# Performance work log

Measured on AMD Instinct MI355X. Metric: run time of the kernel, lower is better.

Reference implementation:

```python
import jax, jax.numpy as jnp
import numpy as np

B, N, D, H = 1, 4096, 512, 8
HD = D // H


def setup_inputs() -> dict:
    key = jax.random.key(0)
    ks = jax.random.split(key, 12)
    s = 0.02  # weight init scale for numerical stability
    query = jax.random.normal(ks[0], (B, N, D), jnp.float32)
    key_t = jax.random.normal(ks[1], (B, N, D), jnp.float32)
    value = jax.random.normal(ks[2], (B, N, D), jnp.float32)
    Wq = jax.random.normal(ks[3], (D, D), jnp.float32) * s
    bq = jax.random.normal(ks[4], (D,), jnp.float32) * s
    Wk = jax.random.normal(ks[5], (D, D), jnp.float32) * s
    bk = jax.random.normal(ks[6], (D,), jnp.float32) * s
    Wv = jax.random.normal(ks[7], (D, D), jnp.float32) * s
    bv = jax.random.normal(ks[8], (D,), jnp.float32) * s
    Wo = jax.random.normal(ks[9], (D, D), jnp.float32) * s
    bo = jax.random.normal(ks[10], (D,), jnp.float32) * s
    # build sgconv_mat exactly as __init__: shifted nonneg adjacency, max-normalized,
    # then symmetric degree normalization D^-1/2 A D^-1/2 (gwmha_layer_num=1)
    A = jax.random.uniform(ks[11], (N, N), jnp.float32)
    A = A + A.min()
    A = A / A.max()
    deg = A.sum(1)
    dinv = 1.0 / jnp.sqrt(deg)
    sgconv_mat = (dinv[:, None] * A * dinv[None, :])[None]  # [1,N,N]
    return {"query": query, "key": key_t, "value": value,
            "Wq": Wq, "bq": bq, "Wk": Wk, "bk": bk, "Wv": Wv, "bv": bv,
            "Wo": Wo, "bo": bo, "sgconv_mat": sgconv_mat}


def reference(query, key, value, Wq, bq, Wk, bk, Wv, bv, Wo, bo, sgconv_mat):
    b, n, d = query.shape
    q = (query @ Wq.T + bq).reshape(b, n, H, HD)
    k = (key @ Wk.T + bk).reshape(b, n, H, HD)
    v = (value @ Wv.T + bv).reshape(b, n, H, HD)
    energy = jnp.einsum('bqhd,bkhd->bhqk', q, k)
    attn = jax.nn.softmax(energy / jnp.sqrt(jnp.float32(d)), axis=3)
    out = jnp.einsum('bhqk,bkhd->bqhd', attn, v).reshape(b, n, d)
    out = sgconv_mat @ out          # [1,N,N] @ [B,N,D] -> [B,N,D]
    return out @ Wo.T + bo
```

## Files before the change

kernel.cpp:

```cpp
#include <hip/hip_runtime.h>
#include <hip/hip_bf16.h>
#include <math.h>

typedef __bf16 bf16_t;
typedef __bf16 bf16x8 __attribute__((ext_vector_type(8)));
typedef unsigned short ushort8v __attribute__((ext_vector_type(8)));
typedef float floatx4 __attribute__((ext_vector_type(4)));

static __device__ inline unsigned short f2bf_rne(float f) {
    unsigned int u = __builtin_bit_cast(unsigned int, f);
    unsigned int r = u + 0x7FFFu + ((u >> 16) & 1u);
    return (unsigned short)(r >> 16);
}
static __device__ inline bf16_t f2bf(float f) {
    return __builtin_bit_cast(bf16_t, f2bf_rne(f));
}

static __device__ inline bf16x8 load8(const bf16_t* p) { return *(const bf16x8*)p; }
static __device__ inline bf16x8 load8(const float* p) {
    float4 a = *(const float4*)p;
    float4 b = *(const float4*)(p + 4);
    ushort8v u;
    u[0] = f2bf_rne(a.x); u[1] = f2bf_rne(a.y); u[2] = f2bf_rne(a.z); u[3] = f2bf_rne(a.w);
    u[4] = f2bf_rne(b.x); u[5] = f2bf_rne(b.y); u[6] = f2bf_rne(b.z); u[7] = f2bf_rne(b.w);
    return __builtin_bit_cast(bf16x8, u);
}
static __device__ inline bf16x8 load8sum(const float* p0, const float* p1) {
    float4 a = *(const float4*)p0;       float4 b = *(const float4*)(p0 + 4);
    float4 c = *(const float4*)p1;       float4 d = *(const float4*)(p1 + 4);
    ushort8v u;
    u[0] = f2bf_rne(a.x + c.x); u[1] = f2bf_rne(a.y + c.y);
    u[2] = f2bf_rne(a.z + c.z); u[3] = f2bf_rne(a.w + c.w);
    u[4] = f2bf_rne(b.x + d.x); u[5] = f2bf_rne(b.y + d.y);
    u[6] = f2bf_rne(b.z + d.z); u[7] = f2bf_rne(b.w + d.w);
    return __builtin_bit_cast(bf16x8, u);
}

static __device__ inline void store_c(float* C, size_t i, float v) { C[i] = v; }
static __device__ inline void store_c(bf16_t* C, size_t i, float v) { C[i] = f2bf(v); }

template <bool ASUM, typename TA, typename TB, typename TC>
__device__ inline void gemm_body(
    const TA* __restrict__ A, const float* __restrict__ A2, int lda,
    const TB* __restrict__ B, int ldb,
    const float* __restrict__ bias_col, const float* __restrict__ bias_row,
    TC* __restrict__ C, int ldc, int K, int m0, int n0)
{
    __shared__ bf16_t As[128 * 40];
    __shared__ bf16_t Bs[64 * 40];

    const int tid = threadIdx.x;
    const int lane = tid & 63, wave = tid >> 6;
    const int wm = wave & 1, wn = wave >> 1;
    const int lo16 = lane & 15, quad = lane >> 4;
    const int sr = tid >> 2, sc = (tid & 3) * 8;

    floatx4 acc[4][2] = {};

    for (int k0 = 0; k0 < K; k0 += 32) {
        bf16x8 a0, a1, b0;
        const size_t ia0 = (size_t)(m0 + sr) * lda + k0 + sc;
        const size_t ia1 = (size_t)(m0 + 64 + sr) * lda + k0 + sc;
        if (ASUM) {
            a0 = load8sum((const float*)A + ia0, A2 + ia0);
            a1 = load8sum((const float*)A + ia1, A2 + ia1);
        } else {
            a0 = load8(A + ia0);
            a1 = load8(A + ia1);
        }
        b0 = load8(B + (size_t)(n0 + sr) * ldb + k0 + sc);
        __syncthreads();
        *(bf16x8*)(&As[sr * 40 + sc]) = a0;
        *(bf16x8*)(&As[(64 + sr) * 40 + sc]) = a1;
        *(bf16x8*)(&Bs[sr * 40 + sc]) = b0;
        __syncthreads();

        bf16x8 af[4], bfv[2];
#pragma unroll
        for (int mt = 0; mt < 4; ++mt)
            af[mt] = *(const bf16x8*)(&As[(wm * 64 + mt * 16 + lo16) * 40 + quad * 8]);
#pragma unroll
        for (int nt = 0; nt < 2; ++nt)
            bfv[nt] = *(const bf16x8*)(&Bs[(wn * 32 + nt * 16 + lo16) * 40 + quad * 8]);
#pragma unroll
        for (int mt = 0; mt < 4; ++mt)
#pragma unroll
            for (int nt = 0; nt < 2; ++nt)
                acc[mt][nt] = __builtin_amdgcn_mfma_f32_16x16x32_bf16(
                    af[mt], bfv[nt], acc[mt][nt], 0, 0, 0);
    }

#pragma unroll
    for (int nt = 0; nt < 2; ++nt) {
        const int gn = n0 + wn * 32 + nt * 16 + lo16;
        const float bc = bias_col ? bias_col[gn] : 0.f;
#pragma unroll
        for (int mt = 0; mt < 4; ++mt) {
#pragma unroll
            for (int r = 0; r < 4; ++r) {
                const int gm = m0 + wm * 64 + mt * 16 + quad * 4 + r;
                float v = acc[mt][nt][r] + bc;
                if (bias_row) v += bias_row[gm];
                store_c(C, (size_t)gm * ldc + gn, v);
            }
        }
    }
}

__global__ __launch_bounds__(256) void proj_qkv(
    const float* __restrict__ query, const float* __restrict__ Wq, const float* __restrict__ bq,
    const float* __restrict__ key,   const float* __restrict__ Wk, const float* __restrict__ bk,
    const float* __restrict__ Wv,    const float* __restrict__ value, const float* __restrict__ bv,
    bf16_t* __restrict__ q, bf16_t* __restrict__ k, bf16_t* __restrict__ vt)
{
    const int b = blockIdx.x;
    const float *A, *B, *bc = nullptr, *br = nullptr;
    bf16_t* C;
    int ldc = 512, m0, n0;
    if (b < 512) {
        int i = b & 255, x = i & 7, t = i >> 3;
        n0 = (t & 7) * 64;
        m0 = ((t >> 3) * 8 + x) * 128;
        if (b < 256) { A = query; B = Wq; bc = bq; C = q; }
        else         { A = key;   B = Wk; bc = bk; C = k; }
    } else {
        int i = b - 512;
        n0 = (i & 63) * 64;
        m0 = (i >> 6) * 128;
        A = Wv; B = value; br = bv; C = vt; ldc = 4096;
    }
    gemm_body<false, float, float, bf16_t>(A, nullptr, 512, B, 512, bc, br, C, ldc, 512, m0, n0);
}

__global__ __launch_bounds__(256) void sgconv_gemm(
    const float* __restrict__ sg, const bf16_t* __restrict__ aot, float* __restrict__ part)
{
    const int b = blockIdx.x;
    const int kb = b >> 8;
    const int i = b & 255, x = i & 7, t = i >> 3;
    const int n0 = (t & 7) * 64, m0 = ((t >> 3) * 8 + x) * 128;
    gemm_body<false, float, bf16_t, float>(
        sg + kb * 2048, nullptr, 4096, aot + kb * 2048, 4096,
        nullptr, nullptr, part + (size_t)kb * 4096 * 512, 512, 2048, m0, n0);
}

__global__ __launch_bounds__(256) void out_proj(
    const float* __restrict__ p0, const float* __restrict__ p1,
    const float* __restrict__ Wo, const float* __restrict__ bo, float* __restrict__ out)
{
    const int i = blockIdx.x, x = i & 7, t = i >> 3;
    const int n0 = (t & 7) * 64, m0 = ((t >> 3) * 8 + x) * 128;
    gemm_body<true, float, float, float>(p0, p1, 512, Wo, 512, bo, nullptr, out, 512, 512, m0, n0);
}

__global__ __launch_bounds__(256, 4) void flash_attn(
    const bf16_t* __restrict__ q, const bf16_t* __restrict__ kk,
    const bf16_t* __restrict__ vt, float* __restrict__ op,
    float* __restrict__ lp, float scale)
{
    const int N = 4096, D = 512;
    const int h   = blockIdx.x & 7;
    const int qb  = (blockIdx.x >> 3) & 31;
    const int qtr = blockIdx.x >> 8;
    const int t0  = qtr * 1024;

    const int tid = threadIdx.x;
    const int w = tid >> 6, lane = tid & 63;
    const int lo16 = lane & 15, quad = lane >> 4;

    __shared__ bf16_t Ks[64 * 72];
    __shared__ bf16_t Vs[64 * 72];
    __shared__ bf16_t Ps[4][32 * 72];

    const bf16_t* qp = q + (size_t)(qb * 128 + w * 32 + lo16) * D + h * 64 + quad * 8;
    bf16x8 qf[2][2];
    qf[0][0] = *(const bf16x8*)qp;
    qf[0][1] = *(const bf16x8*)(qp + 32);
    qf[1][0] = *(const bf16x8*)(qp + 16 * D);
    qf[1][1] = *(const bf16x8*)(qp + 16 * D + 32);

    const int srow = tid >> 2, sc = (tid & 3) * 16;
    const bf16_t* ksrc = kk + (size_t)(t0 + srow) * D + h * 64 + sc;
    const bf16_t* vsrc = vt + (size_t)(h * 64 + srow) * N + t0 + sc;
    bf16_t* kdst = &Ks[srow * 72 + sc];
    bf16_t* vdst = &Vs[srow * 72 + sc];

    floatx4 o[4][2] = {};
    float l[2] = {0.f, 0.f};

    bf16x8 kr0 = *(const bf16x8*)ksrc;
    bf16x8 kr1 = *(const bf16x8*)(ksrc + 8);
    bf16x8 vr0 = *(const bf16x8*)vsrc;
    bf16x8 vr1 = *(const bf16x8*)(vsrc + 8);

    for (int it = 0; it < 16; ++it) {
        __syncthreads();
        *(bf16x8*)kdst = kr0;  *(bf16x8*)(kdst + 8) = kr1;
        *(bf16x8*)vdst = vr0;  *(bf16x8*)(vdst + 8) = vr1;
        __syncthreads();
        if (it < 15) {
            const bf16_t* kn = ksrc + (size_t)(it + 1) * 64 * D;
            const bf16_t* vn = vsrc + (it + 1) * 64;
            kr0 = *(const bf16x8*)kn;  kr1 = *(const bf16x8*)(kn + 8);
            vr0 = *(const bf16x8*)vn;  vr1 = *(const bf16x8*)(vn + 8);
        }

        floatx4 s[4][2];
#pragma unroll
        for (int tt = 0; tt < 4; ++tt) {
            bf16x8 kf0 = *(const bf16x8*)(&Ks[(tt * 16 + lo16) * 72 + quad * 8]);
            bf16x8 kf1 = *(const bf16x8*)(&Ks[(tt * 16 + lo16) * 72 + 32 + quad * 8]);
#pragma unroll
            for (int qt = 0; qt < 2; ++qt) {
                floatx4 a = {};
                a = __builtin_amdgcn_mfma_f32_16x16x32_bf16(kf0, qf[qt][0], a, 0, 0, 0);
                a = __builtin_amdgcn_mfma_f32_16x16x32_bf16(kf1, qf[qt][1], a, 0, 0, 0);
                s[tt][qt] = a;
            }
        }
#pragma unroll
        for (int tt = 0; tt < 4; ++tt)
#pragma unroll
            for (int qt = 0; qt < 2; ++qt) {
                float e0 = __expf(s[tt][qt][0] * scale);
                float e1 = __expf(s[tt][qt][1] * scale);
                float e2 = __expf(s[tt][qt][2] * scale);
                float e3 = __expf(s[tt][qt][3] * scale);
                l[qt] += (e0 + e1) + (e2 + e3);
                uint2 pk;
                pk.x = (unsigned)f2bf_rne(e0) | ((unsigned)f2bf_rne(e1) << 16);
                pk.y = (unsigned)f2bf_rne(e2) | ((unsigned)f2bf_rne(e3) << 16);
                *(uint2*)(&Ps[w][(qt * 16 + lo16) * 72 + tt * 16 + quad * 4]) = pk;
            }
#pragma unroll
        for (int ks = 0; ks < 2; ++ks) {
            bf16x8 pf0 = *(const bf16x8*)(&Ps[w][lo16 * 72 + ks * 32 + quad * 8]);
            bf16x8 pf1 = *(const bf16x8*)(&Ps[w][(16 + lo16) * 72 + ks * 32 + quad * 8]);
#pragma unroll
            for (int t = 0; t < 4; ++t) {
                bf16x8 vf = *(const bf16x8*)(&Vs[(t * 16 + lo16) * 72 + ks * 32 + quad * 8]);
                o[t][0] = __builtin_amdgcn_mfma_f32_16x16x32_bf16(vf, pf0, o[t][0], 0, 0, 0);
                o[t][1] = __builtin_amdgcn_mfma_f32_16x16x32_bf16(vf, pf1, o[t][1], 0, 0, 0);
            }
        }
    }

#pragma unroll
    for (int qt = 0; qt < 2; ++qt) {
        l[qt] += __shfl_xor(l[qt], 16);
        l[qt] += __shfl_xor(l[qt], 32);
    }

    const int g = blockIdx.x & 255;
    float* opw = op + ((size_t)qtr * 256 + g) * 8192;
#pragma unroll
    for (int t = 0; t < 4; ++t)
#pragma unroll
        for (int pt = 0; pt < 2; ++pt)
#pragma unroll
            for (int r = 0; r < 4; ++r)
                opw[(t * 16 + quad * 4 + r) * 128 + w * 32 + pt * 16 + lo16] = o[t][pt][r];

    if (quad == 0) {
        float* lpw = lp + ((size_t)qtr * 256 + g) * 128;
        lpw[w * 32 + lo16] = l[0];
        lpw[w * 32 + 16 + lo16] = l[1];
    }
}

__global__ __launch_bounds__(256) void attn_combine(
    const float* __restrict__ op, const float* __restrict__ lp, bf16_t* __restrict__ aot)
{
    const int g = blockIdx.x;
    const int h = g & 7, qb = g >> 3;
    const int tid = threadIdx.x;
    __shared__ float ls[128];
    if (tid < 128) {
        float s = 0.f;
#pragma unroll
        for (int qtr = 0; qtr < 4; ++qtr)
            s += lp[((size_t)qtr * 256 + g) * 128 + tid];
        ls[tid] = 1.0f / s;
    }
    __syncthreads();
    const float* b0 = op + (size_t)g * 8192;
    const size_t QS = (size_t)256 * 8192;
#pragma unroll 4
    for (int i = 0; i < 32; ++i) {
        int idx = i * 256 + tid;
        float v = b0[idx] + b0[QS + idx] + b0[2 * QS + idx] + b0[3 * QS + idx];
        int dim = idx >> 7, qc = idx & 127;
        aot[(size_t)(h * 64 + dim) * 4096 + qb * 128 + qc] = f2bf(v * ls[qc]);
    }
}

extern "C" void kernel_launch(void* const* d_in, const int* in_sizes, int n_in,
                              void* d_out, int out_size, void* d_ws, size_t ws_size,
                              hipStream_t stream)
{
    const int N = 4096, D = 512;
    const float* query = (const float*)d_in[0];
    const float* key_t = (const float*)d_in[1];
    const float* value = (const float*)d_in[2];
    const float* Wq = (const float*)d_in[3];
    const float* bq = (const float*)d_in[4];
    const float* Wk = (const float*)d_in[5];
    const float* bk = (const float*)d_in[6];
    const float* Wv = (const float*)d_in[7];
    const float* bv = (const float*)d_in[8];
    const float* Wo = (const float*)d_in[9];
    const float* bo = (const float*)d_in[10];
    const float* sg = (const float*)d_in[11];
    float* out = (float*)d_out;

    bf16_t* q   = (bf16_t*)d_ws;
    bf16_t* kk  = q   + (size_t)N * D;
    bf16_t* vt  = kk  + (size_t)N * D;
    bf16_t* aot = vt  + (size_t)N * D;
    float*  op  = (float*)(aot + (size_t)N * D);
    float*  lp  = op + (size_t)4 * 256 * 8192;
    float*  p0  = op;
    float*  p1  = op + (size_t)N * D;

    const dim3 blk(256);

    proj_qkv<<<768, blk, 0, stream>>>(query, Wq, bq, key_t, Wk, bk, Wv, value, bv, q, kk, vt);

    const float scale = 1.0f / sqrtf((float)D);
    flash_attn<<<1024, blk, 0, stream>>>(q, kk, vt, op, lp, scale);
    attn_combine<<<256, blk, 0, stream>>>(op, lp, aot);

    sgconv_gemm<<<512, blk, 0, stream>>>(sg, aot, p0);
    out_proj<<<256, blk, 0, stream>>>(p0, p1, Wo, bo, out);

    (void)in_sizes; (void)n_in; (void)out_size; (void)ws_size;
}
```

Measured before the change: 299.7 us.

## Pre-convert sgconv matrix to bf16 and retile sgconv GEMM with 4-way split-K

The fp32 sgconv matrix is converted to bf16 by 256 extra blocks appended to the projection launch, so the sgconv GEMM reads half the bytes and skips per-tile conversion. The sgconv GEMM gets its own 128x128 tile kernel with 4-way split-K over 1024-wide chunks, replacing the 128x64 tile with 2-way split. The output projection sums four partial buffers, and the LDS row padding goes from 40 to 68 elements. This trades an extra 64MB-read/32MB-write conversion pass and a wider partial-sum reduction for better reuse and fewer bytes in the big GEMM.

```diff
diff --git a/kernel.cpp b/kernel.cpp
--- a/kernel.cpp
+++ b/kernel.cpp
@@ -25,29 +25,35 @@
     u[4] = f2bf_rne(b.x); u[5] = f2bf_rne(b.y); u[6] = f2bf_rne(b.z); u[7] = f2bf_rne(b.w);
     return __builtin_bit_cast(bf16x8, u);
 }
-static __device__ inline bf16x8 load8sum(const float* p0, const float* p1) {
-    float4 a = *(const float4*)p0;       float4 b = *(const float4*)(p0 + 4);
-    float4 c = *(const float4*)p1;       float4 d = *(const float4*)(p1 + 4);
+static __device__ inline bf16x8 load8sum4(const float* p, size_t s) {
+    float4 a0 = *(const float4*)p,           a1 = *(const float4*)(p + 4);
+    float4 b0 = *(const float4*)(p + s),     b1 = *(const float4*)(p + s + 4);
+    float4 c0 = *(const float4*)(p + 2 * s), c1 = *(const float4*)(p + 2 * s + 4);
+    float4 d0 = *(const float4*)(p + 3 * s), d1 = *(const float4*)(p + 3 * s + 4);
     ushort8v u;
-    u[0] = f2bf_rne(a.x + c.x); u[1] = f2bf_rne(a.y + c.y);
-    u[2] = f2bf_rne(a.z + c.z); u[3] = f2bf_rne(a.w + c.w);
-    u[4] = f2bf_rne(b.x + d.x); u[5] = f2bf_rne(b.y + d.y);
-    u[6] = f2bf_rne(b.z + d.z); u[7] = f2bf_rne(b.w + d.w);
+    u[0] = f2bf_rne((a0.x + b0.x) + (c0.x + d0.x));
+    u[1] = f2bf_rne((a0.y + b0.y) + (c0.y + d0.y));
+    u[2] = f2bf_rne((a0.z + b0.z) + (c0.z + d0.z));
+    u[3] = f2bf_rne((a0.w + b0.w) + (c0.w + d0.w));
+    u[4] = f2bf_rne((a1.x + b1.x) + (c1.x + d1.x));
+    u[5] = f2bf_rne((a1.y + b1.y) + (c1.y + d1.y));
+    u[6] = f2bf_rne((a1.z + b1.z) + (c1.z + d1.z));
+    u[7] = f2bf_rne((a1.w + b1.w) + (c1.w + d1.w));
     return __builtin_bit_cast(bf16x8, u);
 }
 
 static __device__ inline void store_c(float* C, size_t i, float v) { C[i] = v; }
 static __device__ inline void store_c(bf16_t* C, size_t i, float v) { C[i] = f2bf(v); }
 
-template <bool ASUM, typename TA, typename TB, typename TC>
+template <int AMODE, typename TA, typename TB, typename TC>
 __device__ inline void gemm_body(
-    const TA* __restrict__ A, const float* __restrict__ A2, int lda,
+    const TA* __restrict__ A, size_t astride, int lda,
     const TB* __restrict__ B, int ldb,
     const float* __restrict__ bias_col, const float* __restrict__ bias_row,
     TC* __restrict__ C, int ldc, int K, int m0, int n0)
 {
-    __shared__ bf16_t As[128 * 40];
-    __shared__ bf16_t Bs[64 * 40];
+    __shared__ bf16_t As[128 * 68];
+    __shared__ bf16_t Bs[64 * 68];
 
     const int tid = threadIdx.x;
     const int lane = tid & 63, wave = tid >> 6;
@@ -61,27 +67,27 @@
         bf16x8 a0, a1, b0;
         const size_t ia0 = (size_t)(m0 + sr) * lda + k0 + sc;
         const size_t ia1 = (size_t)(m0 + 64 + sr) * lda + k0 + sc;
-        if (ASUM) {
-            a0 = load8sum((const float*)A + ia0, A2 + ia0);
-            a1 = load8sum((const float*)A + ia1, A2 + ia1);
+        if (AMODE == 1) {
+            a0 = load8sum4((const float*)A + ia0, astride);
+            a1 = load8sum4((const float*)A + ia1, astride);
         } else {
             a0 = load8(A + ia0);
             a1 = load8(A + ia1);
         }
         b0 = load8(B + (size_t)(n0 + sr) * ldb + k0 + sc);
         __syncthreads();
-        *(bf16x8*)(&As[sr * 40 + sc]) = a0;
-        *(bf16x8*)(&As[(64 + sr) * 40 + sc]) = a1;
-        *(bf16x8*)(&Bs[sr * 40 + sc]) = b0;
+        *(bf16x8*)(&As[sr * 68 + sc]) = a0;
+        *(bf16x8*)(&As[(64 + sr) * 68 + sc]) = a1;
+        *(bf16x8*)(&Bs[sr * 68 + sc]) = b0;
         __syncthreads();
 
         bf16x8 af[4], bfv[2];
 #pragma unroll
         for (int mt = 0; mt < 4; ++mt)
-            af[mt] = *(const bf16x8*)(&As[(wm * 64 + mt * 16 + lo16) * 40 + quad * 8]);
+            af[mt] = *(const bf16x8*)(&As[(wm * 64 + mt * 16 + lo16) * 68 + quad * 8]);
 #pragma unroll
         for (int nt = 0; nt < 2; ++nt)
-            bfv[nt] = *(const bf16x8*)(&Bs[(wn * 32 + nt * 16 + lo16) * 40 + quad * 8]);
+            bfv[nt] = *(const bf16x8*)(&Bs[(wn * 32 + nt * 16 + lo16) * 68 + quad * 8]);
 #pragma unroll
         for (int mt = 0; mt < 4; ++mt)
 #pragma unroll
@@ -111,9 +117,24 @@
     const float* __restrict__ query, const float* __restrict__ Wq, const float* __restrict__ bq,
     const float* __restrict__ key,   const float* __restrict__ Wk, const float* __restrict__ bk,
     const float* __restrict__ Wv,    const float* __restrict__ value, const float* __restrict__ bv,
+    const float* __restrict__ sg,    bf16_t* __restrict__ sgb,
     bf16_t* __restrict__ q, bf16_t* __restrict__ k, bf16_t* __restrict__ vt)
 {
     const int b = blockIdx.x;
+    if (b >= 768) {
+        const size_t base = (size_t)(b - 768) * 65536 + threadIdx.x * 8;
+#pragma unroll 4
+        for (int it = 0; it < 32; ++it) {
+            const size_t idx = base + (size_t)it * 2048;
+            float4 a = *(const float4*)(sg + idx);
+            float4 c = *(const float4*)(sg + idx + 4);
+            ushort8v u;
+            u[0] = f2bf_rne(a.x); u[1] = f2bf_rne(a.y); u[2] = f2bf_rne(a.z); u[3] = f2bf_rne(a.w);
+            u[4] = f2bf_rne(c.x); u[5] = f2bf_rne(c.y); u[6] = f2bf_rne(c.z); u[7] = f2bf_rne(c.w);
+            *(ushort8v*)(sgb + idx) = u;
+        }
+        return;
+    }
     const float *A, *B, *bc = nullptr, *br = nullptr;
     bf16_t* C;
     int ldc = 512, m0, n0;
@@ -129,28 +150,80 @@
         m0 = (i >> 6) * 128;
         A = Wv; B = value; br = bv; C = vt; ldc = 4096;
     }
-    gemm_body<false, float, float, bf16_t>(A, nullptr, 512, B, 512, bc, br, C, ldc, 512, m0, n0);
+    gemm_body<0, float, float, bf16_t>(A, 0, 512, B, 512, bc, br, C, ldc, 512, m0, n0);
 }
 
 __global__ __launch_bounds__(256) void sgconv_gemm(
-    const float* __restrict__ sg, const bf16_t* __restrict__ aot, float* __restrict__ part)
-{
-    const int b = blockIdx.x;
-    const int kb = b >> 8;
-    const int i = b & 255, x = i & 7, t = i >> 3;
-    const int n0 = (t & 7) * 64, m0 = ((t >> 3) * 8 + x) * 128;
-    gemm_body<false, float, bf16_t, float>(
-        sg + kb * 2048, nullptr, 4096, aot + kb * 2048, 4096,
-        nullptr, nullptr, part + (size_t)kb * 4096 * 512, 512, 2048, m0, n0);
+    const bf16_t* __restrict__ sgb, const bf16_t* __restrict__ aot,
+    float* __restrict__ part)
+{
+    const int i = blockIdx.x & 127;
+    const int kb = blockIdx.x >> 7;
+    const int ms = i & 31, ns = i >> 5;
+    const int m0 = ms * 128, n0 = ns * 128;
+    const int kbase = kb * 1024;
+
+    __shared__ bf16_t As[128 * 68];
+    __shared__ bf16_t Bs[128 * 68];
+
+    const int tid = threadIdx.x;
+    const int lane = tid & 63, wave = tid >> 6;
+    const int wm = wave & 1, wn = wave >> 1;
+    const int lo16 = lane & 15, quad = lane >> 4;
+    const int sr = tid >> 1, sc = (tid & 1) * 16;
+
+    const bf16_t* asrc = sgb + (size_t)(m0 + sr) * 4096 + kbase + sc;
+    const bf16_t* bsrc = aot + (size_t)(n0 + sr) * 4096 + kbase + sc;
+
+    floatx4 acc[4][4] = {};
+
+    for (int k0 = 0; k0 < 1024; k0 += 32) {
+        bf16x8 a0 = *(const bf16x8*)(asrc + k0);
+        bf16x8 a1 = *(const bf16x8*)(asrc + k0 + 8);
+        bf16x8 b0 = *(const bf16x8*)(bsrc + k0);
+        bf16x8 b1 = *(const bf16x8*)(bsrc + k0 + 8);
+        __syncthreads();
+        *(bf16x8*)(&As[sr * 68 + sc]) = a0;
+        *(bf16x8*)(&As[sr * 68 + sc + 8]) = a1;
+        *(bf16x8*)(&Bs[sr * 68 + sc]) = b0;
+        *(bf16x8*)(&Bs[sr * 68 + sc + 8]) = b1;
+        __syncthreads();
+
+        bf16x8 af[4], bfv[4];
+#pragma unroll
+        for (int mt = 0; mt < 4; ++mt)
+            af[mt] = *(const bf16x8*)(&As[(wm * 64 + mt * 16 + lo16) * 68 + quad * 8]);
+#pragma unroll
+        for (int nt = 0; nt < 4; ++nt)
+            bfv[nt] = *(const bf16x8*)(&Bs[(wn * 64 + nt * 16 + lo16) * 68 + quad * 8]);
+#pragma unroll
+        for (int mt = 0; mt < 4; ++mt)
+#pragma unroll
+            for (int nt = 0; nt < 4; ++nt)
+                acc[mt][nt] = __builtin_amdgcn_mfma_f32_16x16x32_bf16(
+                    af[mt], bfv[nt], acc[mt][nt], 0, 0, 0);
+    }
+
+    float* pw = part + (size_t)kb * (4096 * 512);
+#pragma unroll
+    for (int mt = 0; mt < 4; ++mt)
+#pragma unroll
+        for (int r = 0; r < 4; ++r) {
+            const int gm = m0 + wm * 64 + mt * 16 + quad * 4 + r;
+#pragma unroll
+            for (int nt = 0; nt < 4; ++nt)
+                pw[(size_t)gm * 512 + n0 + wn * 64 + nt * 16 + lo16] = acc[mt][nt][r];
+        }
 }
 
 __global__ __launch_bounds__(256) void out_proj(
-    const float* __restrict__ p0, const float* __restrict__ p1,
-    const float* __restrict__ Wo, const float* __restrict__ bo, float* __restrict__ out)
+    const float* __restrict__ p, const float* __restrict__ Wo,
+    const float* __restrict__ bo, float* __restrict__ out)
 {
     const int i = blockIdx.x, x = i & 7, t = i >> 3;
     const int n0 = (t & 7) * 64, m0 = ((t >> 3) * 8 + x) * 128;
-    gemm_body<true, float, float, float>(p0, p1, 512, Wo, 512, bo, nullptr, out, 512, 512, m0, n0);
+    gemm_body<1, float, float, float>(p, (size_t)4096 * 512, 512, Wo, 512,
+                                      bo, nullptr, out, 512, 512, m0, n0);
 }
 
 __global__ __launch_bounds__(256, 4) void flash_attn(
@@ -319,19 +392,20 @@
     bf16_t* aot = vt  + (size_t)N * D;
     float*  op  = (float*)(aot + (size_t)N * D);
     float*  lp  = op + (size_t)4 * 256 * 8192;
-    float*  p0  = op;
-    float*  p1  = op + (size_t)N * D;
+    bf16_t* sgb = (bf16_t*)(lp + (size_t)4 * 256 * 128);
+    float*  p   = op;
 
     const dim3 blk(256);
 
-    proj_qkv<<<768, blk, 0, stream>>>(query, Wq, bq, key_t, Wk, bk, Wv, value, bv, q, kk, vt);
+    proj_qkv<<<1024, blk, 0, stream>>>(query, Wq, bq, key_t, Wk, bk,
+                                       Wv, value, bv, sg, sgb, q, kk, vt);
 
     const float scale = 1.0f / sqrtf((float)D);
     flash_attn<<<1024, blk, 0, stream>>>(q, kk, vt, op, lp, scale);
     attn_combine<<<256, blk, 0, stream>>>(op, lp, aot);
 
-    sgconv_gemm<<<512, blk, 0, stream>>>(sg, aot, p0);
-    out_proj<<<256, blk, 0, stream>>>(p0, p1, Wo, bo, out);
+    sgconv_gemm<<<512, blk, 0, stream>>>(sgb, aot, p);
+    out_proj<<<256, blk, 0, stream>>>(p, Wo, bo, out);
 
     (void)in_sizes; (void)n_in; (void)out_size; (void)ws_size;
 }
```

After: 280.6 us. 6.4% less time.
